# Kernel tuning notes

Hardware: AMD Instinct MI355X
Metric: run time of the kernel (lower is better)

The kernel has to match this reference:

```python
import jax, jax.numpy as jnp
import numpy as np

N = 30000   # nodes
E = 150000  # edges per graph
IN = 512
HID = 512
OUT = 256
G = 3


def setup_inputs() -> dict:
    key = jax.random.key(0)
    ks = jax.random.split(key, 16)
    inp = {"x": jax.random.normal(ks[0], (N, IN), jnp.float32)}
    for i in range(G):
        inp[f"edges{i}"] = jax.random.randint(ks[1 + i], (2, E), 0, N)
        inp[f"W{i}"] = jax.random.normal(ks[4 + i], (IN, HID), jnp.float32) / np.sqrt(IN)
        inp[f"b{i}"] = jnp.zeros((HID,), jnp.float32)
    inp["alphas"] = jnp.ones((G,), jnp.float32)
    inp["W_lin"] = jax.random.normal(ks[8], (HID * G, OUT), jnp.float32) / np.sqrt(HID * G)
    inp["b_lin"] = jnp.zeros((OUT,), jnp.float32)
    return inp


def graph_conv(edges, x, W, b):
    # DGL GraphConv, norm='both': out = D_in^{-1/2} A D_out^{-1/2} (X W) + b
    src, dst = edges[0], edges[1]
    ones = jnp.ones(edges.shape[1], x.dtype)
    deg_out = jnp.clip(jax.ops.segment_sum(ones, src, num_segments=N), 1.0)  # out-degree of src nodes
    deg_in = jnp.clip(jax.ops.segment_sum(ones, dst, num_segments=N), 1.0)   # in-degree of dst nodes
    h = (x * jax.lax.rsqrt(deg_out)[:, None]) @ W        # [N, HID] mult-W-first (in_dim >= hid_dim)
    agg = jax.ops.segment_sum(h[src], dst, num_segments=N)  # SpMM via gather + scatter-add
    return agg * jax.lax.rsqrt(deg_in)[:, None] + b


def reference(x, edges0, edges1, edges2, W0, W1, W2, b0, b1, b2, alphas, W_lin, b_lin):
    a = jax.nn.softmax(alphas)  # softmax over the n_graphs axis
    branches = [(edges0, W0, b0), (edges1, W1, b1), (edges2, W2, b2)]
    hs = [jnp.tanh(a[i] * graph_conv(e, x, W, b)) for i, (e, W, b) in enumerate(branches)]
    h = jnp.concatenate(hs, axis=1)  # [N, G*HID]; dropout(p=0) is identity
    return h @ W_lin + b_lin
```

## Files before the change

kernel.cpp:

```cpp
#include <hip/hip_runtime.h>

#define NN 30000
#define NE 150000
#define KIN 512
#define KHID 512
#define KOUT 256
#define NG 3
#define KCAT (KHID*NG)
#define MTILES ((NN + 127) / 128)

typedef __attribute__((ext_vector_type(8))) __bf16 bf16x8;
typedef __attribute__((ext_vector_type(4))) float  f32x4;
typedef __attribute__((ext_vector_type(8))) unsigned short u16x8;

__device__ __forceinline__ unsigned short f2bf(float f) {
    unsigned u = __float_as_uint(f);
    u = (u + 0x7FFFu + ((u >> 16) & 1u)) >> 16;
    return (unsigned short)u;
}
__device__ __forceinline__ float bf2f(unsigned short u) {
    return __uint_as_float((unsigned)u << 16);
}
__device__ __forceinline__ void gl_lds16(const void* g, void* l) {
    __builtin_amdgcn_global_load_lds(
        (const __attribute__((address_space(1))) void*)g,
        (__attribute__((address_space(3))) void*)l, 16, 0, 0);
}

__global__ void k_count(const int* __restrict__ e0, const int* __restrict__ e1,
                        const int* __restrict__ e2, int* cnt_out, int* cnt_in) {
    int idx = blockIdx.x * 256 + threadIdx.x;
    if (idx >= NG * NE) return;
    int g = idx / NE, e = idx - g * NE;
    const int* ed = (g == 0) ? e0 : ((g == 1) ? e1 : e2);
    atomicAdd(&cnt_out[g * NN + ed[e]], 1);
    atomicAdd(&cnt_in [g * NN + ed[NE + e]], 1);
}

__global__ void k_rs(const int* cnt_out, const int* cnt_in, float* rs_out, float* rs_in) {
    int idx = blockIdx.x * 256 + threadIdx.x;
    if (idx >= NG * NN) return;
    int co = cnt_out[idx]; if (co < 1) co = 1;
    int ci = cnt_in [idx]; if (ci < 1) ci = 1;
    rs_out[idx] = rsqrtf((float)co);
    rs_in [idx] = rsqrtf((float)ci);
}

__global__ void k_scan(const int* __restrict__ cnt_in, int* __restrict__ row_off) {
    int g = blockIdx.x;
    const int* c = cnt_in + g * NN;
    int* ro = row_off + g * (NN + 1);
    __shared__ int wsum[16];
    int tid = threadIdx.x, lane = tid & 63, wid = tid >> 6;
    int base = 0;
    for (int start = 0; start < NN; start += 1024) {
        int i = start + tid;
        int v = (i < NN) ? c[i] : 0;
        int inc = v;
        #pragma unroll
        for (int o = 1; o < 64; o <<= 1) {
            int n = __shfl_up(inc, o, 64);
            if (lane >= o) inc += n;
        }
        if (lane == 63) wsum[wid] = inc;
        __syncthreads();
        int wb = 0;
        for (int k = 0; k < wid; k++) wb += wsum[k];
        if (i < NN) ro[i] = base + wb + inc - v;
        int tot = 0;
        for (int k = 0; k < 16; k++) tot += wsum[k];
        base += tot;
        __syncthreads();
    }
    if (tid == 0) ro[NN] = base;
}

__global__ void k_fill(const int* __restrict__ e0, const int* __restrict__ e1,
                       const int* __restrict__ e2, const int* __restrict__ row_off,
                       int* cursor, int* __restrict__ csr) {
    int idx = blockIdx.x * 256 + threadIdx.x;
    if (idx >= NG * NE) return;
    int g = idx / NE, e = idx - g * NE;
    const int* ed = (g == 0) ? e0 : ((g == 1) ? e1 : e2);
    int s = ed[e], d = ed[NE + e];
    int pos = atomicAdd(&cursor[g * NN + d], 1);
    csr[g * NE + row_off[g * (NN + 1) + d] + pos] = s;
}

__global__ void k_misc(const float* __restrict__ alphas,
                       const float* __restrict__ b0, const float* __restrict__ b1,
                       const float* __restrict__ b2, float* __restrict__ aptr,
                       float* __restrict__ bcat) {
    int idx = blockIdx.x * 256 + threadIdx.x;
    if (idx < NG * KHID) {
        int g = idx >> 9;
        const float* b = (g == 0) ? b0 : ((g == 1) ? b1 : b2);
        bcat[idx] = b[idx & 511];
    }
    if (idx == 0) {
        float m = fmaxf(alphas[0], fmaxf(alphas[1], alphas[2]));
        float ex0 = expf(alphas[0] - m), ex1 = expf(alphas[1] - m), ex2 = expf(alphas[2] - m);
        float s = ex0 + ex1 + ex2;
        aptr[0] = ex0 / s; aptr[1] = ex1 / s; aptr[2] = ex2 / s;
    }
}

__global__ __launch_bounds__(256) void k_wt(const float* __restrict__ W0,
        const float* __restrict__ W1, const float* __restrict__ W2,
        const float* __restrict__ Wlin,
        unsigned short* __restrict__ Wt, unsigned short* __restrict__ Wlt) {
    __shared__ float Ls[32][33];
    int bid = blockIdx.x;
    const float* src; unsigned short* dst; int ncols, kdim, k0, n0;
    if (bid < NG * 256) {
        int g = bid >> 8, t = bid & 255;
        int kt = t >> 4, nt = t & 15;
        src = (g == 0) ? W0 : ((g == 1) ? W1 : W2);
        dst = Wt + (size_t)g * KIN * KHID;
        ncols = KHID; kdim = KIN; k0 = kt * 32; n0 = nt * 32;
    } else {
        int t = bid - NG * 256;
        int kt = t % 48, nt = t / 48;
        src = Wlin; dst = Wlt; ncols = KOUT; kdim = KCAT; k0 = kt * 32; n0 = nt * 32;
    }
    int tid = threadIdx.x;
    int r = tid >> 3, c4 = (tid & 7) * 4;
    float4 v = *(const float4*)(src + (size_t)(k0 + r) * ncols + n0 + c4);
    Ls[r][c4 + 0] = v.x; Ls[r][c4 + 1] = v.y; Ls[r][c4 + 2] = v.z; Ls[r][c4 + 3] = v.w;
    __syncthreads();
    int nr = tid >> 3, kc = (tid & 7) * 4;
    ushort4 o;
    o.x = f2bf(Ls[kc + 0][nr]); o.y = f2bf(Ls[kc + 1][nr]);
    o.z = f2bf(Ls[kc + 2][nr]); o.w = f2bf(Ls[kc + 3][nr]);
    *(ushort4*)(dst + (size_t)(n0 + nr) * kdim + k0 + kc) = o;
}

__global__ void k_xbf(const float* __restrict__ x, unsigned short* __restrict__ xb) {
    size_t i = ((size_t)blockIdx.x * 256 + threadIdx.x) * 8;
    float4 v0 = *(const float4*)(x + i);
    float4 v1 = *(const float4*)(x + i + 4);
    uint4 pk;
    pk.x = (unsigned)f2bf(v0.x) | ((unsigned)f2bf(v0.y) << 16);
    pk.y = (unsigned)f2bf(v0.z) | ((unsigned)f2bf(v0.w) << 16);
    pk.z = (unsigned)f2bf(v1.x) | ((unsigned)f2bf(v1.y) << 16);
    pk.w = (unsigned)f2bf(v1.z) | ((unsigned)f2bf(v1.w) << 16);
    *(uint4*)(xb + i) = pk;
}

__global__ __launch_bounds__(256) void k_agg_bf(const unsigned short* __restrict__ xb,
        const int* __restrict__ csr, const int* __restrict__ row_off,
        const float* __restrict__ rs_out, const float* __restrict__ rs_in,
        unsigned short* __restrict__ y, size_t ystride, int gbase) {
    int g    = gbase + blockIdx.z;
    int d    = blockIdx.x * 4 + (threadIdx.x >> 6);
    int lane = threadIdx.x & 63;
    int beg = row_off[g * (NN + 1) + d];
    int end = row_off[g * (NN + 1) + d + 1];
    const int* cs = csr + g * NE;
    float a0=0,a1=0,a2=0,a3=0,a4=0,a5=0,a6=0,a7=0;
    const unsigned short* xbl = xb + lane * 8;
    for (int e = beg; e < end; e++) {
        int s = cs[e];
        float wsc = rs_out[g * NN + s];
        u16x8 v = *(const u16x8*)(xbl + (size_t)s * KIN);
        a0 += wsc * bf2f(v[0]); a1 += wsc * bf2f(v[1]);
        a2 += wsc * bf2f(v[2]); a3 += wsc * bf2f(v[3]);
        a4 += wsc * bf2f(v[4]); a5 += wsc * bf2f(v[5]);
        a6 += wsc * bf2f(v[6]); a7 += wsc * bf2f(v[7]);
    }
    float ri = rs_in[g * NN + d];
    uint4 pk;
    pk.x = (unsigned)f2bf(a0 * ri) | ((unsigned)f2bf(a1 * ri) << 16);
    pk.y = (unsigned)f2bf(a2 * ri) | ((unsigned)f2bf(a3 * ri) << 16);
    pk.z = (unsigned)f2bf(a4 * ri) | ((unsigned)f2bf(a5 * ri) << 16);
    pk.w = (unsigned)f2bf(a6 * ri) | ((unsigned)f2bf(a7 * ri) << 16);
    *(uint4*)(y + (size_t)g * ystride + (size_t)d * KIN + lane * 8) = pk;
}

__global__ __launch_bounds__(256) void k_agg_f32(const float* __restrict__ x,
        const int* __restrict__ csr, const int* __restrict__ row_off,
        const float* __restrict__ rs_out, const float* __restrict__ rs_in,
        unsigned short* __restrict__ y, int g) {
    int d    = blockIdx.x * 4 + (threadIdx.x >> 6);
    int lane = threadIdx.x & 63;
    int beg = row_off[g * (NN + 1) + d];
    int end = row_off[g * (NN + 1) + d + 1];
    const int* cs = csr + g * NE;
    float a0=0,a1=0,a2=0,a3=0,a4=0,a5=0,a6=0,a7=0;
    const float* xb = x + lane * 8;
    for (int e = beg; e < end; e++) {
        int s = cs[e];
        float wsc = rs_out[g * NN + s];
        const float4* xr = (const float4*)(xb + (size_t)s * KIN);
        float4 v0 = xr[0], v1 = xr[1];
        a0 += wsc * v0.x; a1 += wsc * v0.y; a2 += wsc * v0.z; a3 += wsc * v0.w;
        a4 += wsc * v1.x; a5 += wsc * v1.y; a6 += wsc * v1.z; a7 += wsc * v1.w;
    }
    float ri = rs_in[g * NN + d];
    uint4 pk;
    pk.x = (unsigned)f2bf(a0 * ri) | ((unsigned)f2bf(a1 * ri) << 16);
    pk.y = (unsigned)f2bf(a2 * ri) | ((unsigned)f2bf(a3 * ri) << 16);
    pk.z = (unsigned)f2bf(a4 * ri) | ((unsigned)f2bf(a5 * ri) << 16);
    pk.w = (unsigned)f2bf(a6 * ri) | ((unsigned)f2bf(a7 * ri) << 16);
    *(uint4*)(y + (size_t)d * KIN + lane * 8) = pk;
}

template<int KDIM, int NT, bool TANH>
__global__ __launch_bounds__(256) void k_gemm(const unsigned short* __restrict__ A,
        size_t agstride, const unsigned short* __restrict__ Bt,
        const float* __restrict__ bias, const float* __restrict__ aptr, int gbase,
        unsigned short* __restrict__ Tout, float* __restrict__ Fout) {
    constexpr int NF = NT / 32;
    __shared__ __align__(16) unsigned short As[128 * 32];
    __shared__ __align__(16) unsigned short Bs[NT * 32];
    int g = gbase + blockIdx.z;
    const unsigned short* Ab = A + (size_t)g * agstride;
    const unsigned short* Bb = TANH ? (Bt + (size_t)g * KIN * KHID) : Bt;
    const float* bb = TANH ? (bias + g * KHID) : bias;
    int m0 = blockIdx.x * 128;
    int n0 = blockIdx.y * NT;
    int tid = threadIdx.x, lane = tid & 63, w = tid >> 6;

    f32x4 acc[4][NF];
    #pragma unroll
    for (int i = 0; i < 4; i++)
        #pragma unroll
        for (int j = 0; j < NF; j++) acc[i][j] = (f32x4){0.f, 0.f, 0.f, 0.f};

    int mbase = (w & 1) * 64;
    int nbase = (w >> 1) * (NT / 2);
    int mf = mbase + (lane & 15);
    int nf = nbase + (lane & 15);
    int kq = (lane >> 4) * 8;

    int ar0 = tid >> 2, ak0 = (tid & 3) * 8;
    int ar1 = ar0 + 64;
    int ga0 = m0 + ar0; if (ga0 >= NN) ga0 = NN - 1;
    int ga1 = m0 + ar1; if (ga1 >= NN) ga1 = NN - 1;
    const unsigned short* Ag0 = Ab + (size_t)ga0 * KDIM + ak0;
    const unsigned short* Ag1 = Ab + (size_t)ga1 * KDIM + ak0;
    const unsigned short* Bg0 = Bb + (size_t)(n0 + ar0) * KDIM + ak0;
    const unsigned short* Bg1 = Bb + (size_t)(n0 + ar1) * KDIM + ak0;
    unsigned short* Al0 = &As[tid * 8];
    unsigned short* Al1 = &As[(tid + 256) * 8];
    unsigned short* Bl0 = &Bs[tid * 8];
    unsigned short* Bl1 = &Bs[(tid + 256) * 8];

    for (int k0 = 0; k0 < KDIM; k0 += 32) {
        __syncthreads();
        gl_lds16(Ag0 + k0, Al0);
        gl_lds16(Ag1 + k0, Al1);
        gl_lds16(Bg0 + k0, Bl0);
        if constexpr (NT == 128) gl_lds16(Bg1 + k0, Bl1);
        __syncthreads();
        bf16x8 af[4], bfr[NF];
        #pragma unroll
        for (int mi = 0; mi < 4; mi++) af[mi] = *(const bf16x8*)&As[(mf + mi * 16) * 32 + kq];
        #pragma unroll
        for (int ni = 0; ni < NF; ni++) bfr[ni] = *(const bf16x8*)&Bs[(nf + ni * 16) * 32 + kq];
        #pragma unroll
        for (int mi = 0; mi < 4; mi++)
            #pragma unroll
            for (int ni = 0; ni < NF; ni++)
                acc[mi][ni] = __builtin_amdgcn_mfma_f32_16x16x32_bf16(af[mi], bfr[ni], acc[mi][ni], 0, 0, 0);
    }

    float ascale = TANH ? aptr[g] : 0.f;
    int rb = mbase + (lane >> 4) * 4;
    #pragma unroll
    for (int mi = 0; mi < 4; mi++) {
        #pragma unroll
        for (int r = 0; r < 4; r++) {
            int row = m0 + rb + mi * 16 + r;
            if (row < NN) {
                #pragma unroll
                for (int ni = 0; ni < NF; ni++) {
                    int col = n0 + nbase + ni * 16 + (lane & 15);
                    float v = acc[mi][ni][r] + bb[col - n0 + (TANH ? n0 : n0)];
                    v = acc[mi][ni][r] + bb[col];
                    if (TANH) {
                        Tout[(size_t)row * KCAT + g * KHID + col] = f2bf(tanhf(ascale * v));
                    } else {
                        Fout[(size_t)row * KOUT + col] = v;
                    }
                }
            }
        }
    }
}

extern "C" void kernel_launch(void* const* d_in, const int* in_sizes, int n_in,
                              void* d_out, int out_size, void* d_ws, size_t ws_size,
                              hipStream_t stream) {
    const float* x      = (const float*)d_in[0];
    const int*   e0     = (const int*)  d_in[1];
    const float* W0     = (const float*)d_in[2];
    const float* b0     = (const float*)d_in[3];
    const int*   e1     = (const int*)  d_in[4];
    const float* W1     = (const float*)d_in[5];
    const float* b1     = (const float*)d_in[6];
    const int*   e2     = (const int*)  d_in[7];
    const float* W2     = (const float*)d_in[8];
    const float* b2     = (const float*)d_in[9];
    const float* alphas = (const float*)d_in[10];
    const float* Wlin   = (const float*)d_in[11];
    const float* blin   = (const float*)d_in[12];
    float* out = (float*)d_out;

    char* ws = (char*)d_ws;
    size_t off = 0;
    auto alloc = [&](size_t bytes) -> void* {
        void* p = ws + off;
        off = (off + bytes + 255) & ~(size_t)255;
        return p;
    };
    int*   cnt_out = (int*)  alloc((size_t)NG * NN * 4);
    int*   cnt_in  = (int*)  alloc((size_t)NG * NN * 4);
    int*   cursor  = (int*)  alloc((size_t)NG * NN * 4);
    int*   row_off = (int*)  alloc((size_t)NG * (NN + 1) * 4);
    int*   csr     = (int*)  alloc((size_t)NG * NE * 4);
    float* rs_out  = (float*)alloc((size_t)NG * NN * 4);
    float* rs_in   = (float*)alloc((size_t)NG * NN * 4);
    float* aptr    = (float*)alloc(16);
    float* bcat    = (float*)alloc((size_t)NG * KHID * 4);
    unsigned short* Wt  = (unsigned short*)alloc((size_t)NG * KIN * KHID * 2);
    unsigned short* Wlt = (unsigned short*)alloc((size_t)KCAT * KOUT * 2);

    const size_t SZ_Y1 = (size_t)NN * KIN * 2;
    const size_t SZ_T  = (size_t)NN * KCAT * 2;
    size_t remaining = (ws_size > off) ? (ws_size - off) : 0;
    int mode;
    if      (remaining >= 3 * SZ_Y1 + SZ_T + 8192)          mode = 2;
    else if (remaining >= SZ_Y1 + SZ_Y1 + SZ_T + 8192)      mode = 1;
    else                                                    mode = 0;

    unsigned short *y, *xb, *t;
    if (mode == 2) {
        y  = (unsigned short*)alloc(3 * SZ_Y1);
        t  = (unsigned short*)alloc(SZ_T);
        xb = t;
    } else if (mode == 1) {
        y  = (unsigned short*)alloc(SZ_Y1);
        xb = (unsigned short*)alloc(SZ_Y1);
        t  = (unsigned short*)alloc(SZ_T);
    } else {
        y  = (unsigned short*)alloc(SZ_Y1);
        xb = nullptr;
        t  = (unsigned short*)alloc(SZ_T);
    }

    hipMemsetAsync(cnt_out, 0, (size_t)((char*)cursor - (char*)cnt_out) + (size_t)NG * NN * 4, stream);

    k_count<<<(NG * NE + 255) / 256, 256, 0, stream>>>(e0, e1, e2, cnt_out, cnt_in);
    k_rs<<<(NG * NN + 255) / 256, 256, 0, stream>>>(cnt_out, cnt_in, rs_out, rs_in);
    k_scan<<<NG, 1024, 0, stream>>>(cnt_in, row_off);
    k_fill<<<(NG * NE + 255) / 256, 256, 0, stream>>>(e0, e1, e2, row_off, cursor, csr);
    k_misc<<<(NG * KHID + 255) / 256, 256, 0, stream>>>(alphas, b0, b1, b2, aptr, bcat);
    k_wt<<<NG * 256 + 384, 256, 0, stream>>>(W0, W1, W2, Wlin, Wt, Wlt);

    if (mode >= 1) {
        k_xbf<<<NN * KIN / (256 * 8), 256, 0, stream>>>(x, xb);
    }

    if (mode == 2) {
        k_agg_bf<<<dim3(NN / 4, 1, NG), 256, 0, stream>>>(
            xb, csr, row_off, rs_out, rs_in, y, (size_t)NN * KIN, 0);
        k_gemm<KIN, 128, true><<<dim3(MTILES, KHID / 128, NG), 256, 0, stream>>>(
            y, (size_t)NN * KIN, Wt, bcat, aptr, 0, t, nullptr);
    } else {
        for (int g = 0; g < NG; g++) {
            if (mode == 1)
                k_agg_bf<<<dim3(NN / 4, 1, 1), 256, 0, stream>>>(
                    xb, csr, row_off, rs_out, rs_in, y, 0, g);
            else
                k_agg_f32<<<NN / 4, 256, 0, stream>>>(x, csr, row_off, rs_out, rs_in, y, g);
            k_gemm<KIN, 128, true><<<dim3(MTILES, KHID / 128, 1), 256, 0, stream>>>(
                y, 0, Wt, bcat, aptr, g, t, nullptr);
        }
    }
    k_gemm<KCAT, 64, false><<<dim3(MTILES, KOUT / 64, 1), 256, 0, stream>>>(
        t, 0, Wlt, blin, nullptr, 0, nullptr, out);
}
```

Baseline: 479.3 us.

## Double-buffer GEMM LDS tiles, parallelize CSR scan, unroll aggregation, use fast tanh

The GEMM kernel now keeps two LDS buffers and issues the global-to-LDS loads for the next K step before computing on the current one. This removes one barrier per iteration and overlaps load latency with MFMA work. The single-block-per-graph prefix scan becomes a three-kernel chunked scan, the bf16 aggregation loop processes two edges per iteration to keep more gathers in flight, and tanhf is replaced by an exp-based approximation. The cost is twice the LDS per block, which can lower occupancy, plus two extra kernel launches and slightly different tanh rounding.

```diff
diff --git a/kernel.cpp b/kernel.cpp
--- a/kernel.cpp
+++ b/kernel.cpp
@@ -8,6 +8,7 @@
 #define NG 3
 #define KCAT (KHID*NG)
 #define MTILES ((NN + 127) / 128)
+#define NCHUNK 30
 
 typedef __attribute__((ext_vector_type(8))) __bf16 bf16x8;
 typedef __attribute__((ext_vector_type(4))) float  f32x4;
@@ -20,6 +21,10 @@
 }
 __device__ __forceinline__ float bf2f(unsigned short u) {
     return __uint_as_float((unsigned)u << 16);
+}
+__device__ __forceinline__ float fast_tanh(float x) {
+    float e = __expf(2.f * x);
+    return 1.f - __fdividef(2.f, e + 1.f);
 }
 __device__ __forceinline__ void gl_lds16(const void* g, void* l) {
     __builtin_amdgcn_global_load_lds(
@@ -46,33 +51,74 @@
     rs_in [idx] = rsqrtf((float)ci);
 }
 
-__global__ void k_scan(const int* __restrict__ cnt_in, int* __restrict__ row_off) {
-    int g = blockIdx.x;
-    const int* c = cnt_in + g * NN;
+__global__ __launch_bounds__(256) void k_scan1(const int* __restrict__ cnt_in,
+                                               int* __restrict__ csum) {
+    int g = blockIdx.y, c = blockIdx.x;
+    const int* cc = cnt_in + g * NN;
+    int i = c * 1024 + threadIdx.x * 4;
+    int4 v = {0, 0, 0, 0};
+    if (i + 3 < NN) v = *(const int4*)(cc + i);
+    else {
+        if (i     < NN) v.x = cc[i];
+        if (i + 1 < NN) v.y = cc[i + 1];
+        if (i + 2 < NN) v.z = cc[i + 2];
+        if (i + 3 < NN) v.w = cc[i + 3];
+    }
+    int s = v.x + v.y + v.z + v.w;
+    #pragma unroll
+    for (int o = 32; o > 0; o >>= 1) s += __shfl_down(s, o, 64);
+    __shared__ int ws[4];
+    if ((threadIdx.x & 63) == 0) ws[threadIdx.x >> 6] = s;
+    __syncthreads();
+    if (threadIdx.x == 0) csum[g * 32 + c] = ws[0] + ws[1] + ws[2] + ws[3];
+}
+
+__global__ void k_scan2(int* __restrict__ csum) {
+    int g = threadIdx.x >> 6, lane = threadIdx.x & 63;
+    if (g >= NG) return;
+    int v = (lane < NCHUNK) ? csum[g * 32 + lane] : 0;
+    int inc = v;
+    #pragma unroll
+    for (int o = 1; o < 32; o <<= 1) {
+        int n = __shfl_up(inc, o, 64);
+        if (lane >= o) inc += n;
+    }
+    if (lane < NCHUNK) csum[g * 32 + lane] = inc - v;
+}
+
+__global__ __launch_bounds__(256) void k_scan3(const int* __restrict__ cnt_in,
+        const int* __restrict__ csum, int* __restrict__ row_off) {
+    int g = blockIdx.y, c = blockIdx.x;
+    const int* cc = cnt_in + g * NN;
     int* ro = row_off + g * (NN + 1);
-    __shared__ int wsum[16];
-    int tid = threadIdx.x, lane = tid & 63, wid = tid >> 6;
-    int base = 0;
-    for (int start = 0; start < NN; start += 1024) {
-        int i = start + tid;
-        int v = (i < NN) ? c[i] : 0;
-        int inc = v;
-        #pragma unroll
-        for (int o = 1; o < 64; o <<= 1) {
-            int n = __shfl_up(inc, o, 64);
-            if (lane >= o) inc += n;
-        }
-        if (lane == 63) wsum[wid] = inc;
-        __syncthreads();
-        int wb = 0;
-        for (int k = 0; k < wid; k++) wb += wsum[k];
-        if (i < NN) ro[i] = base + wb + inc - v;
-        int tot = 0;
-        for (int k = 0; k < 16; k++) tot += wsum[k];
-        base += tot;
-        __syncthreads();
-    }
-    if (tid == 0) ro[NN] = base;
+    int tid = threadIdx.x, lane = tid & 63, w = tid >> 6;
+    int i = c * 1024 + tid * 4;
+    int4 v = {0, 0, 0, 0};
+    if (i + 3 < NN) v = *(const int4*)(cc + i);
+    else {
+        if (i     < NN) v.x = cc[i];
+        if (i + 1 < NN) v.y = cc[i + 1];
+        if (i + 2 < NN) v.z = cc[i + 2];
+        if (i + 3 < NN) v.w = cc[i + 3];
+    }
+    int s = v.x + v.y + v.z + v.w;
+    int inc = s;
+    #pragma unroll
+    for (int o = 1; o < 64; o <<= 1) {
+        int n = __shfl_up(inc, o, 64);
+        if (lane >= o) inc += n;
+    }
+    __shared__ int ws[4];
+    if (lane == 63) ws[w] = inc;
+    __syncthreads();
+    int base = csum[g * 32 + c];
+    for (int k = 0; k < w; k++) base += ws[k];
+    int excl = base + inc - s;
+    if (i     < NN) ro[i]     = excl;
+    if (i + 1 < NN) ro[i + 1] = excl + v.x;
+    if (i + 2 < NN) ro[i + 2] = excl + v.x + v.y;
+    if (i + 3 < NN) ro[i + 3] = excl + v.x + v.y + v.z;
+    if (c == 0 && tid == 0) ro[NN] = NE;
 }
 
 __global__ void k_fill(const int* __restrict__ e0, const int* __restrict__ e1,
@@ -157,16 +203,32 @@
     int beg = row_off[g * (NN + 1) + d];
     int end = row_off[g * (NN + 1) + d + 1];
     const int* cs = csr + g * NE;
+    const float* rso = rs_out + g * NN;
     float a0=0,a1=0,a2=0,a3=0,a4=0,a5=0,a6=0,a7=0;
     const unsigned short* xbl = xb + lane * 8;
-    for (int e = beg; e < end; e++) {
-        int s = cs[e];
-        float wsc = rs_out[g * NN + s];
-        u16x8 v = *(const u16x8*)(xbl + (size_t)s * KIN);
-        a0 += wsc * bf2f(v[0]); a1 += wsc * bf2f(v[1]);
-        a2 += wsc * bf2f(v[2]); a3 += wsc * bf2f(v[3]);
-        a4 += wsc * bf2f(v[4]); a5 += wsc * bf2f(v[5]);
-        a6 += wsc * bf2f(v[6]); a7 += wsc * bf2f(v[7]);
+    int e = beg;
+    for (; e + 1 < end; e += 2) {
+        int s0 = cs[e], s1 = cs[e + 1];
+        float w0 = rso[s0], w1 = rso[s1];
+        u16x8 v0 = *(const u16x8*)(xbl + (size_t)s0 * KIN);
+        u16x8 v1 = *(const u16x8*)(xbl + (size_t)s1 * KIN);
+        a0 += w0 * bf2f(v0[0]) + w1 * bf2f(v1[0]);
+        a1 += w0 * bf2f(v0[1]) + w1 * bf2f(v1[1]);
+        a2 += w0 * bf2f(v0[2]) + w1 * bf2f(v1[2]);
+        a3 += w0 * bf2f(v0[3]) + w1 * bf2f(v1[3]);
+        a4 += w0 * bf2f(v0[4]) + w1 * bf2f(v1[4]);
+        a5 += w0 * bf2f(v0[5]) + w1 * bf2f(v1[5]);
+        a6 += w0 * bf2f(v0[6]) + w1 * bf2f(v1[6]);
+        a7 += w0 * bf2f(v0[7]) + w1 * bf2f(v1[7]);
+    }
+    if (e < end) {
+        int s0 = cs[e];
+        float w0 = rso[s0];
+        u16x8 v0 = *(const u16x8*)(xbl + (size_t)s0 * KIN);
+        a0 += w0 * bf2f(v0[0]); a1 += w0 * bf2f(v0[1]);
+        a2 += w0 * bf2f(v0[2]); a3 += w0 * bf2f(v0[3]);
+        a4 += w0 * bf2f(v0[4]); a5 += w0 * bf2f(v0[5]);
+        a6 += w0 * bf2f(v0[6]); a7 += w0 * bf2f(v0[7]);
     }
     float ri = rs_in[g * NN + d];
     uint4 pk;
@@ -211,8 +273,9 @@
         const float* __restrict__ bias, const float* __restrict__ aptr, int gbase,
         unsigned short* __restrict__ Tout, float* __restrict__ Fout) {
     constexpr int NF = NT / 32;
-    __shared__ __align__(16) unsigned short As[128 * 32];
-    __shared__ __align__(16) unsigned short Bs[NT * 32];
+    constexpr int NITER = KDIM / 32;
+    __shared__ __align__(16) unsigned short As[2][128 * 32];
+    __shared__ __align__(16) unsigned short Bs[2][NT * 32];
     int g = gbase + blockIdx.z;
     const unsigned short* Ab = A + (size_t)g * agstride;
     const unsigned short* Bb = TANH ? (Bt + (size_t)g * KIN * KHID) : Bt;
@@ -234,30 +297,30 @@
     int kq = (lane >> 4) * 8;
 
     int ar0 = tid >> 2, ak0 = (tid & 3) * 8;
-    int ar1 = ar0 + 64;
-    int ga0 = m0 + ar0; if (ga0 >= NN) ga0 = NN - 1;
-    int ga1 = m0 + ar1; if (ga1 >= NN) ga1 = NN - 1;
+    int ga0 = m0 + ar0;      if (ga0 >= NN) ga0 = NN - 1;
+    int ga1 = m0 + ar0 + 64; if (ga1 >= NN) ga1 = NN - 1;
     const unsigned short* Ag0 = Ab + (size_t)ga0 * KDIM + ak0;
     const unsigned short* Ag1 = Ab + (size_t)ga1 * KDIM + ak0;
     const unsigned short* Bg0 = Bb + (size_t)(n0 + ar0) * KDIM + ak0;
-    const unsigned short* Bg1 = Bb + (size_t)(n0 + ar1) * KDIM + ak0;
-    unsigned short* Al0 = &As[tid * 8];
-    unsigned short* Al1 = &As[(tid + 256) * 8];
-    unsigned short* Bl0 = &Bs[tid * 8];
-    unsigned short* Bl1 = &Bs[(tid + 256) * 8];
-
-    for (int k0 = 0; k0 < KDIM; k0 += 32) {
+    const unsigned short* Bg1 = Bb + (size_t)(n0 + ar0 + 64) * KDIM + ak0;
+
+    auto stage = [&](int buf, int k0) {
+        gl_lds16(Ag0 + k0, &As[buf][tid * 8]);
+        gl_lds16(Ag1 + k0, &As[buf][(tid + 256) * 8]);
+        gl_lds16(Bg0 + k0, &Bs[buf][tid * 8]);
+        if constexpr (NT == 128) gl_lds16(Bg1 + k0, &Bs[buf][(tid + 256) * 8]);
+    };
+    stage(0, 0);
+    for (int it = 0; it < NITER; it++) {
         __syncthreads();
-        gl_lds16(Ag0 + k0, Al0);
-        gl_lds16(Ag1 + k0, Al1);
-        gl_lds16(Bg0 + k0, Bl0);
-        if constexpr (NT == 128) gl_lds16(Bg1 + k0, Bl1);
-        __syncthreads();
+        if (it + 1 < NITER) stage((it + 1) & 1, (it + 1) * 32);
+        const unsigned short* Al = As[it & 1];
+        const unsigned short* Bl = Bs[it & 1];
         bf16x8 af[4], bfr[NF];
         #pragma unroll
-        for (int mi = 0; mi < 4; mi++) af[mi] = *(const bf16x8*)&As[(mf + mi * 16) * 32 + kq];
+        for (int mi = 0; mi < 4; mi++) af[mi] = *(const bf16x8*)&Al[(mf + mi * 16) * 32 + kq];
         #pragma unroll
-        for (int ni = 0; ni < NF; ni++) bfr[ni] = *(const bf16x8*)&Bs[(nf + ni * 16) * 32 + kq];
+        for (int ni = 0; ni < NF; ni++) bfr[ni] = *(const bf16x8*)&Bl[(nf + ni * 16) * 32 + kq];
         #pragma unroll
         for (int mi = 0; mi < 4; mi++)
             #pragma unroll
@@ -276,10 +339,9 @@
                 #pragma unroll
                 for (int ni = 0; ni < NF; ni++) {
                     int col = n0 + nbase + ni * 16 + (lane & 15);
-                    float v = acc[mi][ni][r] + bb[col - n0 + (TANH ? n0 : n0)];
-                    v = acc[mi][ni][r] + bb[col];
+                    float v = acc[mi][ni][r] + bb[col];
                     if (TANH) {
-                        Tout[(size_t)row * KCAT + g * KHID + col] = f2bf(tanhf(ascale * v));
+                        Tout[(size_t)row * KCAT + g * KHID + col] = f2bf(fast_tanh(ascale * v));
                     } else {
                         Fout[(size_t)row * KOUT + col] = v;
                     }
@@ -319,6 +381,7 @@
     int*   cursor  = (int*)  alloc((size_t)NG * NN * 4);
     int*   row_off = (int*)  alloc((size_t)NG * (NN + 1) * 4);
     int*   csr     = (int*)  alloc((size_t)NG * NE * 4);
+    int*   csum    = (int*)  alloc((size_t)NG * 32 * 4);
     float* rs_out  = (float*)alloc((size_t)NG * NN * 4);
     float* rs_in   = (float*)alloc((size_t)NG * NN * 4);
     float* aptr    = (float*)alloc(16);
@@ -353,7 +416,9 @@
 
     k_count<<<(NG * NE + 255) / 256, 256, 0, stream>>>(e0, e1, e2, cnt_out, cnt_in);
     k_rs<<<(NG * NN + 255) / 256, 256, 0, stream>>>(cnt_out, cnt_in, rs_out, rs_in);
-    k_scan<<<NG, 1024, 0, stream>>>(cnt_in, row_off);
+    k_scan1<<<dim3(NCHUNK, NG), 256, 0, stream>>>(cnt_in, csum);
+    k_scan2<<<1, 192, 0, stream>>>(csum);
+    k_scan3<<<dim3(NCHUNK, NG), 256, 0, stream>>>(cnt_in, csum, row_off);
     k_fill<<<(NG * NE + 255) / 256, 256, 0, stream>>>(e0, e1, e2, row_off, cursor, csr);
     k_misc<<<(NG * KHID + 255) / 256, 256, 0, stream>>>(alphas, b0, b1, b2, aptr, bcat);
     k_wt<<<NG * 256 + 384, 256, 0, stream>>>(W0, W1, W2, Wlin, Wt, Wlt);
```

New measurement: 425.7 us. -11.2%, faster.
